# Optimization experiments

Hardware: AMD Instinct MI355X
Metric: run time of the kernel (lower is better)

Reference implementation:

```python
import jax, jax.numpy as jnp
import numpy as np

B, L, D_NODE, D_EDGE, H = 4, 256, 256, 128, 8
DK = D_NODE // H        # 32, per-head node dim
DE = D_EDGE // H        # 16, per-head edge dim
NEG_SLOPE = 0.2

# Static index maps replicating the torch loop indexing (including its j-1 off-by-one / wraparound bug)
_GIDX = np.arange(L - 1)[None, :] + (np.arange(L - 1)[None, :] >= np.arange(L)[:, None])  # [L, L-1]: j-values visited for row i (j != i, in order)
_PIDX = (np.arange(L) - 1) % (L - 1)   # [L]: torch uses attention_probs[:, j-1] for every j != i
_II = np.arange(L)[:, None]            # [L, 1]


def lrelu(x):
    return jnp.where(x >= 0, x, NEG_SLOPE * x)


def setup_inputs() -> dict:
    key = jax.random.key(0)
    ks = jax.random.split(key, 19)
    w = lambda k, s, sc=0.05: jax.random.normal(k, s, jnp.float32) * sc
    return dict(
        node=w(ks[0], (B, L, D_NODE), 1.0),
        edge=w(ks[1], (B, L, L, D_EDGE), 1.0),
        Wn_w=w(ks[2], (D_NODE, D_NODE)), Wn_b=w(ks[3], (D_NODE,)),
        Wh_w=w(ks[4], (DK, DK)), Wh_b=w(ks[5], (DK,)),
        We_w=w(ks[6], (D_EDGE, D_EDGE)), We_b=w(ks[7], (D_EDGE,)),
        Wn2_w=w(ks[8], (D_NODE, D_NODE)), Wn2_b=w(ks[9], (D_NODE,)),
        We2_w=w(ks[10], (D_EDGE, D_EDGE)), We2_b=w(ks[11], (D_EDGE,)),
        attn_w=w(ks[12], (2 * DK + DE,)),                  # attn_linear (no bias), input order [hi, hj, eij]
        edge_w=w(ks[13], (DE + 2 * DK, DE)), edge_b=w(ks[14], (DE,)),  # edge_linear, input order [eij, hi, hj]
        out_n_w=w(ks[15], (D_NODE, D_NODE)), out_n_b=w(ks[16], (D_NODE,)),
        out_e_w=w(ks[17], (D_EDGE, D_EDGE)), out_e_b=w(ks[18], (D_EDGE,)),
    )


def reference(node, edge, Wn_w, Wn_b, Wh_w, Wh_b, We_w, We_b, Wn2_w, Wn2_b,
              We2_w, We2_b, attn_w, edge_w, edge_b, out_n_w, out_n_b, out_e_w, out_e_b):
    node_p = (node @ Wn_w + Wn_b).reshape(B, L, H, DK)
    edge_p = (edge @ We_w + We_b).reshape(B, L, L, H, DE)

    # ---- node update (all heads at once) ----
    wq, wk, we = attn_w[:DK], attn_w[DK:2 * DK], attn_w[2 * DK:]
    si = jnp.einsum('bihd,d->bih', node_p, wq)
    sj = jnp.einsum('bjhd,d->bjh', node_p, wk)
    se = jnp.einsum('bijhd,d->bijh', edge_p, we)
    scores = si[:, :, None, :] + sj[:, None, :, :] + se          # [B,L,L,H], score(i,j)
    sc = scores[:, _II, _GIDX, :]                                 # [B,L,L-1,H]: j != i, loop order
    probs = jax.nn.softmax(lrelu(sc), axis=2)                     # softmax over the L-1 neighbors
    probs_pair = probs[:, :, _PIDX, :]                            # [B,L,L,H]: replicate probs[:, j-1]
    mask = (1.0 - jnp.eye(L, dtype=node.dtype))[None, :, :, None]
    Whh = jnp.einsum('bjhd,de->bjhe', node_p, Wh_w) + Wh_b        # Wh(hj), bias inside the sum
    agg = jnp.einsum('bijh,bjhe->bihe', probs_pair * mask, Whh)
    node_h = (node_p + lrelu(agg)).reshape(B, L, D_NODE)          # concat heads == reshape
    new_node = node_h @ out_n_w + out_n_b

    # ---- edge update ----
    node_p2 = (new_node @ Wn2_w + Wn2_b).reshape(B, L, H, DK)
    edge_p2 = (edge @ We2_w + We2_b).reshape(B, L, L, H, DE)
    w_e, w_i, w_j = edge_w[:DE], edge_w[DE:DE + DK], edge_w[DE + DK:]
    e_new = (jnp.einsum('bijhd,de->bijhe', edge_p2, w_e)
             + jnp.einsum('bihd,de->bihe', node_p2, w_i)[:, :, None]
             + jnp.einsum('bjhd,de->bjhe', node_p2, w_j)[:, None]
             + edge_b)
    e_new = e_new * mask[..., None]                               # diagonal stays zero (zeros_like init)
    new_edge = e_new.reshape(B, L, L, D_EDGE) @ out_e_w + out_e_b
    return new_node, new_edge
```

## Files before the change

kernel.cpp:

```cpp
#include <hip/hip_runtime.h>

#define Bb 4
#define Ll 256
#define NEG 0.2f

typedef __attribute__((ext_vector_type(8))) short short8;
typedef __attribute__((ext_vector_type(4))) float f32x4;
typedef __attribute__((ext_vector_type(4))) unsigned uint4v;

__device__ __forceinline__ float lrelu(float x) { return x >= 0.f ? x : NEG * x; }

__device__ __forceinline__ short f2bf(float x) {
  unsigned u = __builtin_bit_cast(unsigned, x);
  unsigned r = (u + 0x7FFFu + ((u >> 16) & 1u)) >> 16;
  return (short)r;
}

__device__ __forceinline__ unsigned pack2bf(float e, float o) {
  unsigned ue = __builtin_bit_cast(unsigned, e);
  unsigned uo = __builtin_bit_cast(unsigned, o);
  return ((ue + 0x8000u) >> 16) | ((uo + 0x8000u) & 0xFFFF0000u);
}

__global__ void prep_kernel(const float* We_w, const float* We_b, const float* attn_w,
                            const float* We2_w, const float* We2_b, const float* edge_w,
                            const float* edge_b, const float* out_e_w, const float* out_e_b,
                            short* Vbf, float* chg, float* c0g, short* Gsw) {
  int blk = blockIdx.x;
  int t = threadIdx.x;
  if (blk < 128) {
    __shared__ float m2[128];
    int c = blk;
    int h = t >> 4, e = t & 15;
    float s = 0.f;
    for (int d = 0; d < 16; ++d) s += We2_w[c * 128 + h * 16 + d] * edge_w[d * 16 + e];
    m2[t] = s;
    __syncthreads();
    float g = 0.f;
    for (int f = 0; f < 128; ++f) g += m2[f] * out_e_w[f * 128 + t];
    int off = t * 256 + ((2 * c) ^ ((t & 7) << 4));
    *(short*)((char*)Gsw + off) = f2bf(g);
  } else {
    __shared__ float b2e[128];
    const float* we = attn_w + 64;
    for (int idx = t; idx < 1024; idx += 128) {
      int c = idx >> 3, h = idx & 7;
      float s = 0.f;
      for (int d = 0; d < 16; ++d) s += We_w[c * 128 + h * 16 + d] * we[d];
      Vbf[h * 128 + c] = f2bf(s);
      Vbf[(h + 8) * 128 + c] = 0;
    }
    if (t < 8) {
      float s = 0.f;
      for (int d = 0; d < 16; ++d) s += We_b[t * 16 + d] * we[d];
      chg[t] = s;
    }
    {
      int h = t >> 4, e = t & 15;
      float s = 0.f;
      for (int d = 0; d < 16; ++d) s += We2_b[h * 16 + d] * edge_w[d * 16 + e];
      b2e[t] = s + edge_b[e];
    }
    __syncthreads();
    float s = out_e_b[t];
    for (int f = 0; f < 128; ++f) s += b2e[f] * out_e_w[f * 128 + t];
    c0g[t] = s;
  }
}

__global__ __launch_bounds__(256) void se_kernel(const float* __restrict__ edge,
                                                 const short* __restrict__ Vbf,
                                                 const float* __restrict__ chg,
                                                 float* __restrict__ seg) {
  int t = threadIdx.x;
  int w = t >> 6, l = t & 63;
  int lc = l & 15, lq = l >> 4;
  int blk = blockIdx.x;
  long rbase = (long)blk * 128;
  short8 vb[4];
#pragma unroll
  for (int ks = 0; ks < 4; ++ks) vb[ks] = *(const short8*)(Vbf + lc * 128 + ks * 32 + lq * 8);
  float chv = (lc < 8) ? chg[lc] : 0.f;
  int slab = blk >> 1;
  int joff = (blk & 1) * 128;

#pragma unroll
  for (int s = 0; s < 2; ++s) {
    int rowb = w * 32 + s * 16;
    f32x4 acc = (f32x4){0.f, 0.f, 0.f, 0.f};
#pragma unroll
    for (int ks = 0; ks < 4; ++ks) {
      const float* ap = edge + (rbase + rowb + lc) * 128 + ks * 32 + lq * 8;
      float4 f0 = *(const float4*)ap;
      float4 f1 = *(const float4*)(ap + 4);
      uint4v u;
      u.x = pack2bf(f0.x, f0.y);
      u.y = pack2bf(f0.z, f0.w);
      u.z = pack2bf(f1.x, f1.y);
      u.w = pack2bf(f1.z, f1.w);
      acc = __builtin_amdgcn_mfma_f32_16x16x32_bf16(__builtin_bit_cast(short8, u), vb[ks], acc,
                                                    0, 0, 0);
    }
    if (lc < 8) {
#pragma unroll
      for (int r = 0; r < 4; ++r) {
        int row = joff + rowb + lq * 4 + r;
        seg[(long)slab * 2048 + row * 8 + lc] = acc[r] + chv;
      }
    }
  }
}

__global__ __launch_bounds__(256) void node_in_fused(
    const float* __restrict__ node, const float* __restrict__ Wn_w,
    const float* __restrict__ Wn_b, const float* __restrict__ Wh_w,
    const float* __restrict__ Wh_b, const float* __restrict__ attn_w,
    float* __restrict__ node_p, float* __restrict__ Whh, float* __restrict__ si,
    float* __restrict__ sj) {
  __shared__ float a[4][256];
  __shared__ float np[4][256];
  int t = threadIdx.x;
  int row0 = blockIdx.x * 4;
  for (int q = t; q < 1024; q += 256) a[q >> 8][q & 255] = node[(long)row0 * 256 + q];
  __syncthreads();
  float acc[4];
  float bvv = Wn_b[t];
#pragma unroll
  for (int r = 0; r < 4; ++r) acc[r] = bvv;
  for (int k = 0; k < 256; ++k) {
    float w = Wn_w[k * 256 + t];
#pragma unroll
    for (int r = 0; r < 4; ++r) acc[r] += a[r][k] * w;
  }
#pragma unroll
  for (int r = 0; r < 4; ++r) {
    node_p[(long)(row0 + r) * 256 + t] = acc[r];
    np[r][t] = acc[r];
  }
  __syncthreads();
  int h = t >> 5, e = t & 31;
  float wb2 = Wh_b[e];
#pragma unroll
  for (int r = 0; r < 4; ++r) {
    float s = wb2;
    for (int d = 0; d < 32; ++d) s += np[r][h * 32 + d] * Wh_w[d * 32 + e];
    Whh[(long)(row0 + r) * 256 + t] = s;
  }
  if (t < 64) {
    int r = t >> 4, idx = t & 15, hh = idx & 7;
    const float* w = attn_w + (idx < 8 ? 0 : 32);
    float s = 0.f;
    for (int d = 0; d < 32; ++d) s += np[r][hh * 32 + d] * w[d];
    ((idx < 8) ? si : sj)[(long)(row0 + r) * 8 + hh] = s;
  }
}

__global__ __launch_bounds__(256) void attn_fused(
    const float* __restrict__ node_p, const float* __restrict__ Whh,
    const float* __restrict__ si, const float* __restrict__ sj,
    const float* __restrict__ seg, float* __restrict__ node_h) {
  __shared__ float sjl[2048];
  __shared__ float sel[2048];
  __shared__ float pl[2048];
  __shared__ float sil[8];
  int t = threadIdx.x, bi = blockIdx.x;
  int b = bi >> 8, i = bi & 255;
  for (int q = t; q < 2048; q += 256) sjl[q] = sj[(long)b * 2048 + q];
  for (int q = t; q < 2048; q += 256) sel[q] = seg[(long)bi * 2048 + q];
  if (t < 8) sil[t] = si[(long)bi * 8 + t];
  __syncthreads();

  int g = t >> 5, l32 = t & 31;
  float sc[8];
  float mx = -1e30f;
#pragma unroll
  for (int m = 0; m < 8; ++m) {
    int k = l32 + 32 * m;
    float v = -1e30f;
    if (k < 255) {
      int jj = k + (k >= i ? 1 : 0);
      v = sil[g] + sjl[jj * 8 + g] + sel[jj * 8 + g];
      v = lrelu(v);
    }
    sc[m] = v;
    mx = fmaxf(mx, v);
  }
#pragma unroll
  for (int d = 16; d >= 1; d >>= 1) mx = fmaxf(mx, __shfl_xor(mx, d));
  float sum = 0.f;
#pragma unroll
  for (int m = 0; m < 8; ++m) {
    int k = l32 + 32 * m;
    float e = (k < 255) ? __expf(sc[m] - mx) : 0.f;
    sc[m] = e;
    sum += e;
  }
#pragma unroll
  for (int d = 16; d >= 1; d >>= 1) sum += __shfl_xor(sum, d);
  float inv = 1.f / sum;
#pragma unroll
  for (int m = 0; m < 8; ++m) {
    int k = l32 + 32 * m;
    if (k < 255) pl[k * 8 + g] = sc[m] * inv;
  }
  __syncthreads();

  int h = g;
  const float* wb = Whh + (long)b * 65536 + t;
  float acc0 = 0.f, acc1 = 0.f;
#pragma unroll 8
  for (int j = 0; j < 256; j += 2) {
    int k0 = (j == 0) ? 254 : (j - 1);
    int k1 = j;
    float w0 = (j == i) ? 0.f : pl[k0 * 8 + h];
    float w1 = (j + 1 == i) ? 0.f : pl[k1 * 8 + h];
    acc0 += w0 * wb[(long)j * 256];
    acc1 += w1 * wb[(long)(j + 1) * 256];
  }
  float acc = acc0 + acc1;
  float np = node_p[(long)bi * 256 + t];
  node_h[(long)bi * 256 + t] = np + lrelu(acc);
}

__global__ __launch_bounds__(256) void node_out_pq(
    const float* __restrict__ node_h, const float* __restrict__ out_n_w,
    const float* __restrict__ out_n_b, const float* __restrict__ Wn2_w,
    const float* __restrict__ Wn2_b, const float* __restrict__ edge_w,
    const float* __restrict__ out_e_w, float* __restrict__ out_node,
    float* __restrict__ Pg, float* __restrict__ Qg) {
  __shared__ float a[4][256];
  __shared__ float b2[4][256];
  __shared__ float ninj[4][256];
  int t = threadIdx.x;
  int row0 = blockIdx.x * 4;
  for (int q = t; q < 1024; q += 256) a[q >> 8][q & 255] = node_h[(long)row0 * 256 + q];
  __syncthreads();
  float acc[4];
  float bv1 = out_n_b[t];
#pragma unroll
  for (int r = 0; r < 4; ++r) acc[r] = bv1;
  for (int k = 0; k < 256; ++k) {
    float w = out_n_w[k * 256 + t];
#pragma unroll
    for (int r = 0; r < 4; ++r) acc[r] += a[r][k] * w;
  }
#pragma unroll
  for (int r = 0; r < 4; ++r) {
    out_node[(long)(row0 + r) * 256 + t] = acc[r];
    b2[r][t] = acc[r];
  }
  __syncthreads();
  float acc2[4];
  float bv2 = Wn2_b[t];
#pragma unroll
  for (int r = 0; r < 4; ++r) acc2[r] = bv2;
  for (int k = 0; k < 256; ++k) {
    float w = Wn2_w[k * 256 + t];
#pragma unroll
    for (int r = 0; r < 4; ++r) acc2[r] += b2[r][k] * w;
  }
#pragma unroll
  for (int r = 0; r < 4; ++r) a[r][t] = acc2[r];
  __syncthreads();
  {
    int f = t & 127, h = f >> 4, e = f & 15;
    const float* w = edge_w + 256 + (t >> 7) * 512;
#pragma unroll
    for (int r = 0; r < 4; ++r) {
      float s = 0.f;
      for (int d = 0; d < 32; ++d) s += a[r][h * 32 + d] * w[d * 16 + e];
      ninj[r][t] = s;
    }
  }
  __syncthreads();
  {
    int o = t & 127;
    int half = (t >> 7) * 128;
#pragma unroll
    for (int r = 0; r < 4; ++r) {
      float s = 0.f;
      const float* src = ninj[r] + half;
      for (int f = 0; f < 128; ++f) s += src[f] * out_e_w[f * 128 + o];
      ((t < 128) ? Pg : Qg)[(long)(row0 + r) * 128 + o] = s;
    }
  }
}

__global__ __launch_bounds__(256) void edge_out_kernel(
    const float* __restrict__ edge, const short* __restrict__ Gsw,
    const float* __restrict__ Pg, const float* __restrict__ Qg,
    const float* __restrict__ c0g, const float* __restrict__ oeb,
    float* __restrict__ out_edge) {
  __shared__ __align__(16) char Gl[32768];
  int t = threadIdx.x;
  int w = t >> 6, l = t & 63;
  int lc = l & 15, lq = l >> 4;
  int bi = blockIdx.x;
  int b = bi >> 8, i = bi & 255;

  {
    const uint4v* gsrc = (const uint4v*)Gsw;
    uint4v* gdst = (uint4v*)Gl;
#pragma unroll
    for (int q = 0; q < 8; ++q) gdst[q * 256 + t] = gsrc[q * 256 + t];
  }
  float pcv[8], oebv[8];
#pragma unroll
  for (int nf = 0; nf < 8; ++nf) {
    int col = nf * 16 + lc;
    pcv[nf] = Pg[(long)bi * 128 + col] + c0g[col];
    oebv[nf] = oeb[col];
  }
  __syncthreads();

  const float* eslab = edge + (long)bi * 32768;
#pragma unroll
  for (int s = 0; s < 4; ++s) {
    int rowb = w * 64 + s * 16;
    f32x4 acc[8];
#pragma unroll
    for (int nf = 0; nf < 8; ++nf) acc[nf] = (f32x4){0.f, 0.f, 0.f, 0.f};
#pragma unroll
    for (int ks = 0; ks < 4; ++ks) {
      const float* ap = eslab + (long)(rowb + lc) * 128 + ks * 32 + lq * 8;
      float4 f0 = *(const float4*)ap;
      float4 f1 = *(const float4*)(ap + 4);
      uint4v u;
      u.x = pack2bf(f0.x, f0.y);
      u.y = pack2bf(f0.z, f0.w);
      u.z = pack2bf(f1.x, f1.y);
      u.w = pack2bf(f1.z, f1.w);
      short8 av = __builtin_bit_cast(short8, u);
#pragma unroll
      for (int nf = 0; nf < 8; ++nf) {
        int col = nf * 16 + lc;
        short8 bvv =
            *(const short8*)(Gl + col * 256 + ((ks * 64 + lq * 16) ^ ((col & 7) << 4)));
        acc[nf] = __builtin_amdgcn_mfma_f32_16x16x32_bf16(av, bvv, acc[nf], 0, 0, 0);
      }
    }
#pragma unroll
    for (int r = 0; r < 4; ++r) {
      int jloc = rowb + lq * 4 + r;
      float* orow = out_edge + ((long)bi * 256 + jloc) * 128;
      const float* Qrow = Qg + (long)(b * 256 + jloc) * 128;
      bool diag = (jloc == i);
#pragma unroll
      for (int nf = 0; nf < 8; ++nf) {
        int col = nf * 16 + lc;
        float v = diag ? oebv[nf] : (acc[nf][r] + pcv[nf] + Qrow[col]);
        orow[col] = v;
      }
    }
  }
}

extern "C" void kernel_launch(void* const* d_in, const int* in_sizes, int n_in,
                              void* d_out, int out_size, void* d_ws, size_t ws_size,
                              hipStream_t stream) {
  const float* node = (const float*)d_in[0];
  const float* edge = (const float*)d_in[1];
  const float* Wn_w = (const float*)d_in[2];
  const float* Wn_b = (const float*)d_in[3];
  const float* Wh_w = (const float*)d_in[4];
  const float* Wh_b = (const float*)d_in[5];
  const float* We_w = (const float*)d_in[6];
  const float* We_b = (const float*)d_in[7];
  const float* Wn2_w = (const float*)d_in[8];
  const float* Wn2_b = (const float*)d_in[9];
  const float* We2_w = (const float*)d_in[10];
  const float* We2_b = (const float*)d_in[11];
  const float* attn_w = (const float*)d_in[12];
  const float* edge_w = (const float*)d_in[13];
  const float* edge_b = (const float*)d_in[14];
  const float* out_n_w = (const float*)d_in[15];
  const float* out_n_b = (const float*)d_in[16];
  const float* out_e_w = (const float*)d_in[17];
  const float* out_e_b = (const float*)d_in[18];

  float* out_node = (float*)d_out;
  float* out_edge = ((float*)d_out) + 262144;

  float* ws = (float*)d_ws;
  float* node_p = ws;
  float* Whh    = ws + 262144;
  float* node_h = ws + 524288;
  float* si     = ws + 786432;
  float* sjv    = ws + 794624;
  float* Pg     = ws + 802816;
  float* Qg     = ws + 933888;
  float* chg    = ws + 1064960;
  float* c0g    = ws + 1065088;
  short* Gsw    = (short*)(ws + 1065216);
  short* Vbf    = (short*)(ws + 1073408);
  float* seg    = ws + 1074432;

  prep_kernel<<<129, 128, 0, stream>>>(We_w, We_b, attn_w, We2_w, We2_b, edge_w, edge_b,
                                       out_e_w, out_e_b, Vbf, chg, c0g, Gsw);
  node_in_fused<<<256, 256, 0, stream>>>(node, Wn_w, Wn_b, Wh_w, Wh_b, attn_w, node_p, Whh,
                                         si, sjv);
  se_kernel<<<2048, 256, 0, stream>>>(edge, Vbf, chg, seg);
  attn_fused<<<1024, 256, 0, stream>>>(node_p, Whh, si, sjv, seg, node_h);
  node_out_pq<<<256, 256, 0, stream>>>(node_h, out_n_w, out_n_b, Wn2_w, Wn2_b, edge_w,
                                       out_e_w, out_node, Pg, Qg);
  edge_out_kernel<<<1024, 256, 0, stream>>>(edge, Gsw, Pg, Qg, c0g, out_e_b, out_edge);
}
```

Measured before the change: 170.9 us.

## Compute edge scores in fp32 with grid-stride shuffle reduction; split edge_out blocks

Replaces the bf16 MFMA score projection in se_kernel with an fp32 CUDA-core dot product. Each 16-lane group handles one edge row and reduces the 8 head partial sums with a butterfly shuffle inside a grid-stride loop. This avoids bf16 rounding and the half-empty MFMA tiles, at the cost of more VALU work and shuffles. Separately, edge_out_kernel now launches twice as many blocks, each covering half the j range, to raise parallelism, but every block reloads the 32KB G matrix into LDS.

```diff
diff --git a/kernel.cpp b/kernel.cpp
--- a/kernel.cpp
+++ b/kernel.cpp
@@ -25,7 +25,7 @@
 __global__ void prep_kernel(const float* We_w, const float* We_b, const float* attn_w,
                             const float* We2_w, const float* We2_b, const float* edge_w,
                             const float* edge_b, const float* out_e_w, const float* out_e_b,
-                            short* Vbf, float* chg, float* c0g, short* Gsw) {
+                            float* Vg, float* chg, float* c0g, short* Gsw) {
   int blk = blockIdx.x;
   int t = threadIdx.x;
   if (blk < 128) {
@@ -47,8 +47,7 @@
       int c = idx >> 3, h = idx & 7;
       float s = 0.f;
       for (int d = 0; d < 16; ++d) s += We_w[c * 128 + h * 16 + d] * we[d];
-      Vbf[h * 128 + c] = f2bf(s);
-      Vbf[(h + 8) * 128 + c] = 0;
+      Vg[idx] = s;
     }
     if (t < 8) {
       float s = 0.f;
@@ -69,45 +68,52 @@
 }
 
 __global__ __launch_bounds__(256) void se_kernel(const float* __restrict__ edge,
-                                                 const short* __restrict__ Vbf,
+                                                 const float* __restrict__ Vg,
                                                  const float* __restrict__ chg,
-                                                 float* __restrict__ seg) {
+                                                 float* __restrict__ se) {
   int t = threadIdx.x;
-  int w = t >> 6, l = t & 63;
-  int lc = l & 15, lq = l >> 4;
-  int blk = blockIdx.x;
-  long rbase = (long)blk * 128;
-  short8 vb[4];
-#pragma unroll
-  for (int ks = 0; ks < 4; ++ks) vb[ks] = *(const short8*)(Vbf + lc * 128 + ks * 32 + lq * 8);
-  float chv = (lc < 8) ? chg[lc] : 0.f;
-  int slab = blk >> 1;
-  int joff = (blk & 1) * 128;
-
-#pragma unroll
-  for (int s = 0; s < 2; ++s) {
-    int rowb = w * 32 + s * 16;
-    f32x4 acc = (f32x4){0.f, 0.f, 0.f, 0.f};
-#pragma unroll
-    for (int ks = 0; ks < 4; ++ks) {
-      const float* ap = edge + (rbase + rowb + lc) * 128 + ks * 32 + lq * 8;
-      float4 f0 = *(const float4*)ap;
-      float4 f1 = *(const float4*)(ap + 4);
-      uint4v u;
-      u.x = pack2bf(f0.x, f0.y);
-      u.y = pack2bf(f0.z, f0.w);
-      u.z = pack2bf(f1.x, f1.y);
-      u.w = pack2bf(f1.z, f1.w);
-      acc = __builtin_amdgcn_mfma_f32_16x16x32_bf16(__builtin_bit_cast(short8, u), vb[ks], acc,
-                                                    0, 0, 0);
-    }
-    if (lc < 8) {
-#pragma unroll
-      for (int r = 0; r < 4; ++r) {
-        int row = joff + rowb + lq * 4 + r;
-        seg[(long)slab * 2048 + row * 8 + lc] = acc[r] + chv;
-      }
-    }
+  int l16 = t & 15;
+  long gid = ((long)blockIdx.x * 256 + t) >> 4;
+  long ngroups = ((long)gridDim.x * 256) >> 4;
+  float vreg[8][8];
+#pragma unroll
+  for (int ci = 0; ci < 8; ++ci) {
+    int c = (ci < 4) ? (l16 * 4 + ci) : (64 + l16 * 4 + (ci - 4));
+#pragma unroll
+    for (int h = 0; h < 8; ++h) vreg[ci][h] = Vg[c * 8 + h];
+  }
+  float chv = chg[(l16 >> 1) & 7];
+  const long NR = (long)Bb * Ll * Ll;
+  for (long row = gid; row < NR; row += ngroups) {
+    const float4* er = reinterpret_cast<const float4*>(edge + row * 128);
+    float4 e0 = er[l16];
+    float4 e1 = er[16 + l16];
+    float p[8];
+#pragma unroll
+    for (int h = 0; h < 8; ++h)
+      p[h] = e0.x * vreg[0][h] + e0.y * vreg[1][h] + e0.z * vreg[2][h] + e0.w * vreg[3][h] +
+             e1.x * vreg[4][h] + e1.y * vreg[5][h] + e1.z * vreg[6][h] + e1.w * vreg[7][h];
+    bool hi8 = (l16 & 8) != 0;
+    float q[4];
+#pragma unroll
+    for (int h = 0; h < 4; ++h) {
+      float keep = hi8 ? p[h + 4] : p[h];
+      float send = hi8 ? p[h] : p[h + 4];
+      q[h] = keep + __shfl_xor(send, 8);
+    }
+    bool hi4 = (l16 & 4) != 0;
+    float r2[2];
+#pragma unroll
+    for (int h = 0; h < 2; ++h) {
+      float keep = hi4 ? q[h + 2] : q[h];
+      float send = hi4 ? q[h] : q[h + 2];
+      r2[h] = keep + __shfl_xor(send, 4);
+    }
+    bool hi2 = (l16 & 2) != 0;
+    float s = (hi2 ? r2[1] : r2[0]) + __shfl_xor(hi2 ? r2[0] : r2[1], 2);
+    s += __shfl_xor(s, 1);
+    s += chv;
+    if ((l16 & 1) == 0) se[row * 8 + ((l16 >> 1) & 7)] = s;
   }
 }
 
@@ -295,7 +301,9 @@
   int t = threadIdx.x;
   int w = t >> 6, l = t & 63;
   int lc = l & 15, lq = l >> 4;
-  int bi = blockIdx.x;
+  int blk = blockIdx.x;
+  int bi = blk >> 1;
+  int jh = (blk & 1) * 128;
   int b = bi >> 8, i = bi & 255;
 
   {
@@ -315,8 +323,8 @@
 
   const float* eslab = edge + (long)bi * 32768;
 #pragma unroll
-  for (int s = 0; s < 4; ++s) {
-    int rowb = w * 64 + s * 16;
+  for (int s = 0; s < 2; ++s) {
+    int rowb = jh + w * 32 + s * 16;
     f32x4 acc[8];
 #pragma unroll
     for (int nf = 0; nf < 8; ++nf) acc[nf] = (f32x4){0.f, 0.f, 0.f, 0.f};
@@ -392,16 +400,16 @@
   float* chg    = ws + 1064960;
   float* c0g    = ws + 1065088;
   short* Gsw    = (short*)(ws + 1065216);
-  short* Vbf    = (short*)(ws + 1073408);
+  float* Vg     = ws + 1073408;
   float* seg    = ws + 1074432;
 
   prep_kernel<<<129, 128, 0, stream>>>(We_w, We_b, attn_w, We2_w, We2_b, edge_w, edge_b,
-                                       out_e_w, out_e_b, Vbf, chg, c0g, Gsw);
+                                       out_e_w, out_e_b, Vg, chg, c0g, Gsw);
   node_in_fused<<<256, 256, 0, stream>>>(node, Wn_w, Wn_b, Wh_w, Wh_b, attn_w, node_p, Whh,
                                          si, sjv);
-  se_kernel<<<2048, 256, 0, stream>>>(edge, Vbf, chg, seg);
+  se_kernel<<<2048, 256, 0, stream>>>(edge, Vg, chg, seg);
   attn_fused<<<1024, 256, 0, stream>>>(node_p, Whh, si, sjv, seg, node_h);
   node_out_pq<<<256, 256, 0, stream>>>(node_h, out_n_w, out_n_b, Wn2_w, Wn2_b, edge_w,
                                        out_e_w, out_node, Pg, Qg);
-  edge_out_kernel<<<1024, 256, 0, stream>>>(edge, Gsw, Pg, Qg, c0g, out_e_b, out_edge);
-}
+  edge_out_kernel<<<2048, 256, 0, stream>>>(edge, Gsw, Pg, Qg, c0g, out_e_b, out_edge);
+}
```

After: 167.5 us. 2.0% less time.
